# Optimization experiments

Hardware: AMD Instinct MI355X
Metric: run time of the kernel (lower is better)

The kernel has to match this reference:

```python
import jax, jax.numpy as jnp
import numpy as np

IMAGE_SIZE = 128
PATCH_SIZE = 8
BOND_DIM = 128
CP_RANK = 64
EMBED_DIM = 512
BATCH = 512
GRID = IMAGE_SIZE // PATCH_SIZE            # 16
NUM_PATCHES = GRID * GRID                  # 256
DEPTH = 4                                  # log4(256)
LEVEL_NODES = [64, 16, 4, 1]


def setup_inputs() -> dict:
    key = jax.random.key(0)
    ks = jax.random.split(key, 32)
    s = 0.02
    inp = {
        "x": jax.random.normal(ks[0], (BATCH, 1, IMAGE_SIZE, IMAGE_SIZE), jnp.float32),
        "W_patch": jax.random.normal(ks[1], (PATCH_SIZE * PATCH_SIZE, BOND_DIM), jnp.float32) * s,
        "b_patch": jnp.zeros((BOND_DIM,), jnp.float32),
        "pos": jax.random.normal(ks[2], (1, NUM_PATCHES, BOND_DIM), jnp.float32),
        "gamma": jnp.ones((BOND_DIM,), jnp.float32),
        "beta": jnp.zeros((BOND_DIM,), jnp.float32),
        "W_head": jax.random.normal(ks[3], (BOND_DIM, EMBED_DIM), jnp.float32) * s,
        "b_head": jnp.zeros((EMBED_DIM,), jnp.float32),
    }
    for lvl, n in enumerate(LEVEL_NODES):
        # per-node distinct CP factors: 4 children in_dim->rank, then rank->out_dim
        inp[f"f{lvl}"] = jax.random.normal(ks[4 + 2 * lvl], (n, 4, BOND_DIM, CP_RANK), jnp.float32) * s
        inp[f"o{lvl}"] = jax.random.normal(ks[5 + 2 * lvl], (n, CP_RANK, BOND_DIM), jnp.float32) * s
    return inp


def _patchify(x):
    # 'b c (h p1) (w p2) -> b (h w) (p1 p2 c)', c == 1
    b = x.shape[0]
    x = x.reshape(b, 1, GRID, PATCH_SIZE, GRID, PATCH_SIZE)
    x = x.transpose(0, 2, 4, 3, 5, 1)                  # b h w p1 p2 c
    return x.reshape(b, NUM_PATCHES, PATCH_SIZE * PATCH_SIZE)


def _quad_group(x, grid):
    # 'b (h w) c -> b (h/2 w/2) (h2 w2) c' with 2x2 blocks
    b, _, c = x.shape
    g2 = grid // 2
    x = x.reshape(b, g2, 2, g2, 2, c).transpose(0, 1, 3, 2, 4, 5)
    return x.reshape(b, g2 * g2, 4, c)


def _cp_level(x, f, o):
    # x: [b, n, 4, C]; f: [n, 4, C, R]; o: [n, R, C]
    u = jnp.einsum('bnqc,nqcr->bnqr', x, f)
    p = jnp.prod(u, axis=2)                            # [b, n, R]
    return jnp.einsum('bnr,nrc->bnc', p, o)


def reference(x, W_patch, b_patch, pos, f0, o0, f1, o1, f2, o2, f3, o3,
              gamma, beta, W_head, b_head):
    h = _patchify(x) @ W_patch + b_patch               # [b, 256, C]
    h = h + pos
    grid = GRID
    for f, o in ((f0, o0), (f1, o1), (f2, o2), (f3, o3)):
        h = _cp_level(_quad_group(h, grid), f, o)
        grid //= 2
    h = h[:, 0, :]                                     # squeeze node dim
    mu = jnp.mean(h, axis=-1, keepdims=True)
    var = jnp.var(h, axis=-1, keepdims=True)
    h = (h - mu) / jnp.sqrt(var + 1e-5) * gamma + beta
    out = h @ W_head + b_head
    n = jnp.maximum(jnp.linalg.norm(out, axis=-1, keepdims=True), 1e-12)
    return out / n
```

## Files before the change

kernel.cpp:

```cpp
#include <hip/hip_runtime.h>
#include <hip/hip_bf16.h>

#define BATCH     512
#define IMG       128
#define PS        8
#define GRID_P    16
#define NP        256
#define C         128
#define R         64
#define E         512

typedef float f32x4 __attribute__((ext_vector_type(4)));
typedef short s16x8 __attribute__((ext_vector_type(8)));

__device__ __forceinline__ unsigned short f2bf(float x) {
    unsigned int u = __float_as_uint(x);
    u += 0x7fffu + ((u >> 16) & 1u);
    return (unsigned short)(u >> 16);
}
__device__ __forceinline__ float bf2f(unsigned short h) {
    return __uint_as_float(((unsigned int)h) << 16);
}

__global__ __launch_bounds__(256) void prep_all_kernel(
    const float* __restrict__ f0, const float* __restrict__ f1,
    const float* __restrict__ f2, const float* __restrict__ f3,
    const float* __restrict__ o0, const float* __restrict__ o1,
    const float* __restrict__ o2, const float* __restrict__ o3,
    const float* __restrict__ Wh, const float* __restrict__ Wp,
    const float* __restrict__ pos, const float* __restrict__ bp,
    unsigned short* __restrict__ fTL, unsigned short* __restrict__ oT,
    unsigned short* __restrict__ WhT, unsigned short* __restrict__ WfT,
    float* __restrict__ pf)
{
    __shared__ float ls[128 * 68];
    __shared__ float red[64 * 4];
    const int bi = blockIdx.x, t = threadIdx.x;

    if (bi < 256) {
        const float* src = f0 + (size_t)bi * 8192;
#pragma unroll
        for (int i = 0; i < 8; ++i) {
            const int fi = (t + 256 * i) * 4;
            const int c = fi >> 6, r = fi & 63;
            *(float4*)(ls + c * 68 + r) = *(const float4*)(src + fi);
        }
        __syncthreads();

        const int w = t >> 6, lane = t & 63;
        const int m = lane & 15, g = lane >> 4;

        f32x4 acc[4];
#pragma unroll
        for (int nt = 0; nt < 4; ++nt) acc[nt] = (f32x4){0.f, 0.f, 0.f, 0.f};
#pragma unroll
        for (int kt = 0; kt < 4; ++kt) {
            s16x8 afr;
#pragma unroll
            for (int e = 0; e < 8; ++e)
                afr[e] = (short)f2bf(ls[(kt * 32 + g * 8 + e) * 68 + w * 16 + m]);
#pragma unroll
            for (int nt = 0; nt < 4; ++nt) {
                const float* wr = Wp + (size_t)(nt * 16 + m) * 128 + kt * 32 + g * 8;
                const float4 b0 = *(const float4*)wr;
                const float4 b1 = *(const float4*)(wr + 4);
                s16x8 bfr;
                bfr[0] = (short)f2bf(b0.x); bfr[1] = (short)f2bf(b0.y);
                bfr[2] = (short)f2bf(b0.z); bfr[3] = (short)f2bf(b0.w);
                bfr[4] = (short)f2bf(b1.x); bfr[5] = (short)f2bf(b1.y);
                bfr[6] = (short)f2bf(b1.z); bfr[7] = (short)f2bf(b1.w);
                acc[nt] = __builtin_amdgcn_mfma_f32_16x16x32_bf16(afr, bfr, acc[nt], 0, 0, 0);
            }
        }
        unsigned short* D = WfT + (size_t)bi * 4096;
#pragma unroll
        for (int nt = 0; nt < 4; ++nt)
#pragma unroll
            for (int j = 0; j < 4; ++j)
                D[(size_t)(w * 16 + g * 4 + j) * 64 + nt * 16 + m] = f2bf(acc[nt][j]);

        {
            const int r = t & 63, half = t >> 6;
            const int n0 = bi >> 2, q = bi & 3;
            const int pp = (2 * (n0 >> 3) + (q >> 1)) * GRID_P + 2 * (n0 & 7) + (q & 1);
            const float* posr = pos + (size_t)pp * C;
            float s = 0.f;
#pragma unroll 8
            for (int e = 0; e < 32; ++e) {
                const int c = half * 32 + e;
                s += (posr[c] + bp[c]) * ls[c * 68 + r];
            }
            red[r * 4 + half] = s;
        }
        __syncthreads();
        if (t < 64)
            pf[bi * 64 + t] = red[t * 4 + 0] + red[t * 4 + 1] + red[t * 4 + 2] + red[t * 4 + 3];
    } else if (bi < 340) {
        const int ti = bi - 256;
        const float* src;
        if      (ti < 64) src = f1 + (size_t)ti * 8192;
        else if (ti < 80) src = f2 + (size_t)(ti - 64) * 8192;
        else              src = f3 + (size_t)(ti - 80) * 8192;
        unsigned short* dst = fTL + (size_t)ti * 8192;
#pragma unroll
        for (int i = 0; i < 8; ++i) {
            const int fi = (t + 256 * i) * 4;
            const int c = fi >> 6, r = fi & 63;
            *(float4*)(ls + c * 68 + r) = *(const float4*)(src + fi);
        }
        __syncthreads();
        const int rr = t >> 2, seg = t & 3;
        unsigned int* d32 = (unsigned int*)(dst + rr * 128 + seg * 32);
#pragma unroll
        for (int ii = 0; ii < 16; ++ii) {
            const int c = seg * 32 + ii * 2;
            const unsigned int lo = f2bf(ls[c * 68 + rr]);
            const unsigned int hi = f2bf(ls[(c + 1) * 68 + rr]);
            d32[ii] = lo | (hi << 16);
        }
    } else if (bi < 425) {
        const int oi = bi - 340;
        const float* src;
        if      (oi < 64) src = o0 + (size_t)oi * 8192;
        else if (oi < 80) src = o1 + (size_t)(oi - 64) * 8192;
        else if (oi < 84) src = o2 + (size_t)(oi - 80) * 8192;
        else              src = o3 + (size_t)(oi - 84) * 8192;
        unsigned short* dst = oT + (size_t)oi * 8192;
#pragma unroll
        for (int i = 0; i < 8; ++i) {
            const int fi = (t + 256 * i) * 4;
            const int r = fi >> 7, c = fi & 127;
            *(float4*)(ls + r * 132 + c) = *(const float4*)(src + fi);
        }
        __syncthreads();
        const int cc = t >> 1, seg = t & 1;
        unsigned int* d32 = (unsigned int*)(dst + cc * 64 + seg * 32);
#pragma unroll
        for (int ii = 0; ii < 16; ++ii) {
            const int r = seg * 32 + ii * 2;
            const unsigned int lo = f2bf(ls[r * 132 + cc]);
            const unsigned int hi = f2bf(ls[(r + 1) * 132 + cc]);
            d32[ii] = lo | (hi << 16);
        }
    } else {
        const int j = bi - 425;
#pragma unroll
        for (int i = 0; i < 8; ++i) {
            const int fi = (t + 256 * i) * 4;
            const int c = fi >> 6, e = fi & 63;
            *(float4*)(ls + c * 68 + e) = *(const float4*)(Wh + (size_t)c * E + j * 64 + e);
        }
        __syncthreads();
        const int rr = t >> 2, seg = t & 3;
        unsigned int* d32 = (unsigned int*)(WhT + (size_t)(j * 64 + rr) * 128 + seg * 32);
#pragma unroll
        for (int ii = 0; ii < 16; ++ii) {
            const int c = seg * 32 + ii * 2;
            const unsigned int lo = f2bf(ls[c * 68 + rr]);
            const unsigned int hi = f2bf(ls[(c + 1) * 68 + rr]);
            d32[ii] = lo | (hi << 16);
        }
    }
}

__global__ __launch_bounds__(256, 3) void level01_fused(
    const float* __restrict__ x,
    const unsigned short* __restrict__ WfT,
    const float* __restrict__ pf,
    const unsigned short* __restrict__ oT,
    const unsigned short* __restrict__ fT1,
    unsigned short* __restrict__ h2)
{
    __shared__ __align__(16) float          us1[4 * 16 * 68];
    __shared__ __align__(16) unsigned short ps0[4 * 16 * 72];
    __shared__ __align__(16) unsigned short ps1[16 * 72];
    __shared__ __align__(16) unsigned short h1s[4 * 16 * 136];

    const int bi = blockIdx.x;
    const int n1 = bi >> 5, btile = bi & 31;
    const int t = threadIdx.x, w = t >> 6, lane = t & 63;
    const int m = lane & 15, g = lane >> 4;
    const int bt = btile * 16;

    const int y1g = n1 >> 2, x1g = n1 & 3;
    const int Ry0 = y1g * 32, Rx0 = x1g * 32;
    const int n0 = (2 * y1g + (w >> 1)) * 8 + 2 * x1g + (w & 1);

    s16x8 a[4][2];
    {
        const int rbase = 16 * (w >> 1);
        const int cbase = 16 * (w & 1);
        const float* xb = x + (size_t)(bt + m) * (IMG * IMG);
#pragma unroll
        for (int q = 0; q < 4; ++q) {
            const int rq = rbase + 8 * (q >> 1) + g;
            const int cc = cbase + 8 * (q & 1);
#pragma unroll
            for (int kt = 0; kt < 2; ++kt) {
                const float* px = xb + (size_t)(Ry0 + rq + kt * 4) * IMG + Rx0 + cc;
                const float4 p0 = *(const float4*)px;
                const float4 p1 = *(const float4*)(px + 4);
                s16x8 fr;
                fr[0] = (short)f2bf(p0.x); fr[1] = (short)f2bf(p0.y);
                fr[2] = (short)f2bf(p0.z); fr[3] = (short)f2bf(p0.w);
                fr[4] = (short)f2bf(p1.x); fr[5] = (short)f2bf(p1.y);
                fr[6] = (short)f2bf(p1.z); fr[7] = (short)f2bf(p1.w);
                a[q][kt] = fr;
            }
        }
    }

    f32x4 accu[4][4];
#pragma unroll
    for (int q = 0; q < 4; ++q) {
        const float* pfq = pf + (size_t)(n0 * 4 + q) * 64;
#pragma unroll
        for (int nt = 0; nt < 4; ++nt) {
            const float pv = pfq[nt * 16 + m];
            accu[q][nt] = (f32x4){pv, pv, pv, pv};
        }
    }
#pragma unroll
    for (int q = 0; q < 4; ++q) {
        const unsigned short* Wq = WfT + (size_t)(n0 * 4 + q) * 4096;
#pragma unroll
        for (int kt = 0; kt < 2; ++kt) {
            const int koff = kt * 32 + g * 8;
#pragma unroll
            for (int nt = 0; nt < 4; ++nt) {
                const s16x8 bfr = *(const s16x8*)(Wq + (size_t)(nt * 16 + m) * 64 + koff);
                accu[q][nt] = __builtin_amdgcn_mfma_f32_16x16x32_bf16(a[q][kt], bfr, accu[q][nt], 0, 0, 0);
            }
        }
    }

    unsigned short* myps = ps0 + w * (16 * 72);
#pragma unroll
    for (int nt = 0; nt < 4; ++nt) {
        const f32x4 pr = accu[0][nt] * accu[1][nt] * accu[2][nt] * accu[3][nt];
#pragma unroll
        for (int j = 0; j < 4; ++j)
            myps[(g * 4 + j) * 72 + nt * 16 + m] = f2bf(pr[j]);
    }

    {
        s16x8 ap[2];
#pragma unroll
        for (int kt = 0; kt < 2; ++kt)
            ap[kt] = *(const s16x8*)(myps + m * 72 + kt * 32 + g * 8);
        const unsigned short* oTn = oT + (size_t)n0 * 8192;
        unsigned short* myh = h1s + w * (16 * 136);
#pragma unroll
        for (int ct = 0; ct < 8; ++ct) {
            f32x4 aco = (f32x4){0.f, 0.f, 0.f, 0.f};
#pragma unroll
            for (int kt = 0; kt < 2; ++kt) {
                const s16x8 bfr = *(const s16x8*)(oTn + (size_t)(ct * 16 + m) * 64 + kt * 32 + g * 8);
                aco = __builtin_amdgcn_mfma_f32_16x16x32_bf16(ap[kt], bfr, aco, 0, 0, 0);
            }
#pragma unroll
            for (int j = 0; j < 4; ++j)
                myh[(g * 4 + j) * 136 + ct * 16 + m] = f2bf(aco[j]);
        }
    }

    {
        const unsigned short* myh = h1s + w * (16 * 136);
        const unsigned short* fq = fT1 + (size_t)(n1 * 4 + w) * 8192;
        f32x4 au[4];
#pragma unroll
        for (int nt = 0; nt < 4; ++nt) au[nt] = (f32x4){0.f, 0.f, 0.f, 0.f};
#pragma unroll
        for (int kt = 0; kt < 4; ++kt) {
            const int koff = kt * 32 + g * 8;
            const s16x8 afr = *(const s16x8*)(myh + m * 136 + koff);
#pragma unroll
            for (int nt = 0; nt < 4; ++nt) {
                const s16x8 bfr = *(const s16x8*)(fq + (size_t)(nt * 16 + m) * 128 + koff);
                au[nt] = __builtin_amdgcn_mfma_f32_16x16x32_bf16(afr, bfr, au[nt], 0, 0, 0);
            }
        }
#pragma unroll
        for (int nt = 0; nt < 4; ++nt)
#pragma unroll
            for (int j = 0; j < 4; ++j)
                us1[(w * 16 + g * 4 + j) * 68 + nt * 16 + m] = au[nt][j];
    }
    __syncthreads();

    {
        const int pb = t >> 4, r0 = (t & 15) * 4;
        const f32x4 u0 = *(const f32x4*)(us1 + (0 * 16 + pb) * 68 + r0);
        const f32x4 u1 = *(const f32x4*)(us1 + (1 * 16 + pb) * 68 + r0);
        const f32x4 u2 = *(const f32x4*)(us1 + (2 * 16 + pb) * 68 + r0);
        const f32x4 u3 = *(const f32x4*)(us1 + (3 * 16 + pb) * 68 + r0);
        const f32x4 p = u0 * u1 * u2 * u3;
        uint2 v;
        v.x = (unsigned int)f2bf(p[0]) | ((unsigned int)f2bf(p[1]) << 16);
        v.y = (unsigned int)f2bf(p[2]) | ((unsigned int)f2bf(p[3]) << 16);
        *(uint2*)(ps1 + pb * 72 + r0) = v;
    }
    __syncthreads();

    {
        s16x8 ap[2];
#pragma unroll
        for (int kt = 0; kt < 2; ++kt)
            ap[kt] = *(const s16x8*)(ps1 + m * 72 + kt * 32 + g * 8);
        const unsigned short* oTn = oT + (size_t)(64 + n1) * 8192;
#pragma unroll
        for (int i = 0; i < 2; ++i) {
            const int ct = w * 2 + i;
            f32x4 aco = (f32x4){0.f, 0.f, 0.f, 0.f};
#pragma unroll
            for (int kt = 0; kt < 2; ++kt) {
                const s16x8 bfr = *(const s16x8*)(oTn + (size_t)(ct * 16 + m) * 64 + kt * 32 + g * 8);
                aco = __builtin_amdgcn_mfma_f32_16x16x32_bf16(ap[kt], bfr, aco, 0, 0, 0);
            }
#pragma unroll
            for (int j = 0; j < 4; ++j)
                h2[((size_t)(bt + g * 4 + j) * 16 + n1) * C + ct * 16 + m] = f2bf(aco[j]);
        }
    }
}

__global__ __launch_bounds__(256, 1) void tail_kernel(
    const unsigned short* __restrict__ h2,
    const unsigned short* __restrict__ fT2,
    const unsigned short* __restrict__ oT2,
    const unsigned short* __restrict__ fT3,
    const unsigned short* __restrict__ oT3,
    const float* __restrict__ gamma, const float* __restrict__ beta,
    const unsigned short* __restrict__ WhT,
    const float* __restrict__ bh,
    float* __restrict__ out)
{
    __shared__ __align__(16) float          us3[4 * 16 * 68];
    __shared__ __align__(16) unsigned short ps2[4 * 16 * 72];
    __shared__ __align__(16) unsigned short ps3[16 * 72];
    __shared__ __align__(16) unsigned short h3s[16 * 4 * 136];
    __shared__ __align__(16) float          h4s[16 * 132];
    __shared__ __align__(16) unsigned short hns[16 * 136];
    __shared__ float red[16 * 4];

    const int bt = blockIdx.x * 16;
    const int t = threadIdx.x, w = t >> 6, lane = t & 63;
    const int m = lane & 15, g = lane >> 4;

    {
        const int n2 = w;
        const int y1 = n2 >> 1, x1 = n2 & 1;

        s16x8 xa[4][4];
#pragma unroll
        for (int q = 0; q < 4; ++q) {
            const int pidx = (2 * y1 + (q >> 1)) * 4 + 2 * x1 + (q & 1);
            const unsigned short* xq = h2 + ((size_t)(bt + m) * 16 + pidx) * C;
#pragma unroll
            for (int kt = 0; kt < 4; ++kt)
                xa[q][kt] = *(const s16x8*)(xq + kt * 32 + g * 8);
        }

        f32x4 acc_u[4][4];
#pragma unroll
        for (int q = 0; q < 4; ++q)
#pragma unroll
            for (int nt = 0; nt < 4; ++nt) acc_u[q][nt] = (f32x4){0.f, 0.f, 0.f, 0.f};
#pragma unroll
        for (int q = 0; q < 4; ++q) {
            const unsigned short* fq = fT2 + (size_t)(n2 * 4 + q) * R * C;
#pragma unroll
            for (int kt = 0; kt < 4; ++kt) {
                const int koff = kt * 32 + g * 8;
#pragma unroll
                for (int nt = 0; nt < 4; ++nt) {
                    const s16x8 bfr = *(const s16x8*)(fq + (size_t)(nt * 16 + m) * C + koff);
                    acc_u[q][nt] = __builtin_amdgcn_mfma_f32_16x16x32_bf16(xa[q][kt], bfr, acc_u[q][nt], 0, 0, 0);
                }
            }
        }

        s16x8 ob[8][2];
        {
            const unsigned short* oTn = oT2 + (size_t)n2 * C * R;
#pragma unroll
            for (int ct = 0; ct < 8; ++ct)
#pragma unroll
                for (int kt = 0; kt < 2; ++kt)
                    ob[ct][kt] = *(const s16x8*)(oTn + (size_t)(ct * 16 + m) * R + kt * 32 + g * 8);
        }

        unsigned short* myps2 = ps2 + w * 16 * 72;
#pragma unroll
        for (int nt = 0; nt < 4; ++nt) {
            const f32x4 p = acc_u[0][nt] * acc_u[1][nt] * acc_u[2][nt] * acc_u[3][nt];
#pragma unroll
            for (int j = 0; j < 4; ++j)
                myps2[(g * 4 + j) * 72 + nt * 16 + m] = f2bf(p[j]);
        }
        f32x4 aco[8];
#pragma unroll
        for (int ct = 0; ct < 8; ++ct) aco[ct] = (f32x4){0.f, 0.f, 0.f, 0.f};
#pragma unroll
        for (int kt = 0; kt < 2; ++kt) {
            const int koff = kt * 32 + g * 8;
            const s16x8 av = *(const s16x8*)(myps2 + m * 72 + koff);
#pragma unroll
            for (int ct = 0; ct < 8; ++ct)
                aco[ct] = __builtin_amdgcn_mfma_f32_16x16x32_bf16(av, ob[ct][kt], aco[ct], 0, 0, 0);
        }
#pragma unroll
        for (int ct = 0; ct < 8; ++ct)
#pragma unroll
            for (int j = 0; j < 4; ++j)
                h3s[((g * 4 + j) * 4 + n2) * 136 + ct * 16 + m] = f2bf(aco[ct][j]);
    }
    __syncthreads();

    {
        const int q = w;
        s16x8 fb[4][4];
        {
            const unsigned short* fq = fT3 + (size_t)q * R * C;
#pragma unroll
            for (int kt = 0; kt < 4; ++kt)
#pragma unroll
                for (int nt = 0; nt < 4; ++nt)
                    fb[kt][nt] = *(const s16x8*)(fq + (size_t)(nt * 16 + m) * C + kt * 32 + g * 8);
        }
        f32x4 acc_u[4];
#pragma unroll
        for (int nt = 0; nt < 4; ++nt) acc_u[nt] = (f32x4){0.f, 0.f, 0.f, 0.f};
#pragma unroll
        for (int kt = 0; kt < 4; ++kt) {
            const int koff = kt * 32 + g * 8;
            const s16x8 av = *(const s16x8*)(h3s + (m * 4 + q) * 136 + koff);
#pragma unroll
            for (int nt = 0; nt < 4; ++nt)
                acc_u[nt] = __builtin_amdgcn_mfma_f32_16x16x32_bf16(av, fb[kt][nt], acc_u[nt], 0, 0, 0);
        }
#pragma unroll
        for (int nt = 0; nt < 4; ++nt)
#pragma unroll
            for (int j = 0; j < 4; ++j)
                us3[(q * 16 + g * 4 + j) * 68 + nt * 16 + m] = acc_u[nt][j];
    }
    __syncthreads();
    {
        const int pb = t >> 4, r0 = (t & 15) * 4;
        const f32x4 u0 = *(const f32x4*)(us3 + (0 * 16 + pb) * 68 + r0);
        const f32x4 u1 = *(const f32x4*)(us3 + (1 * 16 + pb) * 68 + r0);
        const f32x4 u2 = *(const f32x4*)(us3 + (2 * 16 + pb) * 68 + r0);
        const f32x4 u3 = *(const f32x4*)(us3 + (3 * 16 + pb) * 68 + r0);
        const f32x4 p = u0 * u1 * u2 * u3;
        uint2 v;
        v.x = (unsigned int)f2bf(p[0]) | ((unsigned int)f2bf(p[1]) << 16);
        v.y = (unsigned int)f2bf(p[2]) | ((unsigned int)f2bf(p[3]) << 16);
        *(uint2*)(ps3 + pb * 72 + r0) = v;
    }
    __syncthreads();
    {
        s16x8 ap[2];
#pragma unroll
        for (int kt = 0; kt < 2; ++kt)
            ap[kt] = *(const s16x8*)(ps3 + m * 72 + kt * 32 + g * 8);
#pragma unroll
        for (int i = 0; i < 2; ++i) {
            f32x4 aco = (f32x4){0.f, 0.f, 0.f, 0.f};
            const int ct = w * 2 + i;
#pragma unroll
            for (int kt = 0; kt < 2; ++kt) {
                const s16x8 bfr = *(const s16x8*)(oT3 + (size_t)(ct * 16 + m) * R + kt * 32 + g * 8);
                aco = __builtin_amdgcn_mfma_f32_16x16x32_bf16(ap[kt], bfr, aco, 0, 0, 0);
            }
#pragma unroll
            for (int j = 0; j < 4; ++j)
                h4s[(g * 4 + j) * 132 + ct * 16 + m] = aco[j];
        }
    }
    __syncthreads();

    {
        const int rb = w * 4 + g;
        const int c0 = m * 8;
        const f32x4 v0 = *(const f32x4*)(h4s + rb * 132 + c0);
        const f32x4 v1 = *(const f32x4*)(h4s + rb * 132 + c0 + 4);
        float s  = v0[0] + v0[1] + v0[2] + v0[3] + v1[0] + v1[1] + v1[2] + v1[3];
        float ss = v0[0]*v0[0] + v0[1]*v0[1] + v0[2]*v0[2] + v0[3]*v0[3]
                 + v1[0]*v1[0] + v1[1]*v1[1] + v1[2]*v1[2] + v1[3]*v1[3];
#pragma unroll
        for (int off = 1; off < 16; off <<= 1) {
            s  += __shfl_xor(s, off);
            ss += __shfl_xor(ss, off);
        }
        const float mu   = s * (1.f / C);
        const float var  = ss * (1.f / C) - mu * mu;
        const float rstd = rsqrtf(var + 1e-5f);
        const f32x4 ga0 = *(const f32x4*)(gamma + c0);
        const f32x4 ga1 = *(const f32x4*)(gamma + c0 + 4);
        const f32x4 be0 = *(const f32x4*)(beta + c0);
        const f32x4 be1 = *(const f32x4*)(beta + c0 + 4);
        unsigned int o32[4];
        float hv[8];
#pragma unroll
        for (int k = 0; k < 4; ++k) hv[k]     = (v0[k] - mu) * rstd * ga0[k] + be0[k];
#pragma unroll
        for (int k = 0; k < 4; ++k) hv[4 + k] = (v1[k] - mu) * rstd * ga1[k] + be1[k];
#pragma unroll
        for (int k = 0; k < 4; ++k)
            o32[k] = (unsigned int)f2bf(hv[2*k]) | ((unsigned int)f2bf(hv[2*k+1]) << 16);
        *(uint4*)(hns + rb * 136 + c0) = *(uint4*)o32;
    }
    __syncthreads();

    {
        f32x4 acc[8];
#pragma unroll
        for (int nt = 0; nt < 8; ++nt) {
            const int e = w * 128 + nt * 16 + m;
            const float bv = bh[e];
            acc[nt] = (f32x4){bv, bv, bv, bv};
        }
#pragma unroll
        for (int kt = 0; kt < 4; ++kt) {
            const int koff = kt * 32 + g * 8;
            const s16x8 av = *(const s16x8*)(hns + m * 136 + koff);
#pragma unroll
            for (int nt = 0; nt < 8; ++nt) {
                const int e = w * 128 + nt * 16 + m;
                const s16x8 bfr = *(const s16x8*)(WhT + (size_t)e * 128 + koff);
                acc[nt] = __builtin_amdgcn_mfma_f32_16x16x32_bf16(av, bfr, acc[nt], 0, 0, 0);
            }
        }
        float sq[4];
#pragma unroll
        for (int j = 0; j < 4; ++j) {
            float s = 0.f;
#pragma unroll
            for (int nt = 0; nt < 8; ++nt) s += acc[nt][j] * acc[nt][j];
#pragma unroll
            for (int off = 1; off < 16; off <<= 1) s += __shfl_xor(s, off);
            sq[j] = s;
        }
        if (m == 0) {
#pragma unroll
            for (int j = 0; j < 4; ++j) red[(g * 4 + j) * 4 + w] = sq[j];
        }
        __syncthreads();
#pragma unroll
        for (int j = 0; j < 4; ++j) {
            const int row = g * 4 + j;
            const float tot = red[row * 4 + 0] + red[row * 4 + 1]
                            + red[row * 4 + 2] + red[row * 4 + 3];
            const float inv = 1.f / fmaxf(sqrtf(tot), 1e-12f);
#pragma unroll
            for (int nt = 0; nt < 8; ++nt) {
                const int e = w * 128 + nt * 16 + m;
                out[(size_t)(bt + row) * E + e] = acc[nt][j] * inv;
            }
        }
    }
}

extern "C" void kernel_launch(void* const* d_in, const int* in_sizes, int n_in,
                              void* d_out, int out_size, void* d_ws, size_t ws_size,
                              hipStream_t stream) {
    const float* x     = (const float*)d_in[0];
    const float* Wp    = (const float*)d_in[1];
    const float* bp    = (const float*)d_in[2];
    const float* pos   = (const float*)d_in[3];
    const float* gamma = (const float*)d_in[4];
    const float* beta  = (const float*)d_in[5];
    const float* Wh    = (const float*)d_in[6];
    const float* bh    = (const float*)d_in[7];
    const float* f0    = (const float*)d_in[8];
    const float* o0    = (const float*)d_in[9];
    const float* f1    = (const float*)d_in[10];
    const float* o1    = (const float*)d_in[11];
    const float* f2    = (const float*)d_in[12];
    const float* o2    = (const float*)d_in[13];
    const float* f3    = (const float*)d_in[14];
    const float* o3    = (const float*)d_in[15];
    float* out = (float*)d_out;

    unsigned short* h2  = (unsigned short*)d_ws;
    unsigned short* fTL = h2 + (size_t)1048576;
    unsigned short* oT  = fTL + (size_t)688128;
    unsigned short* WfT = oT + (size_t)696320;
    unsigned short* WhT = WfT + (size_t)1048576;
    float*          pff = (float*)(WhT + 65536);

    unsigned short* fT1 = fTL;
    unsigned short* fT2 = fTL + (size_t)64 * 8192;
    unsigned short* fT3 = fTL + (size_t)80 * 8192;
    unsigned short* oT2 = oT + (size_t)80 * 8192;
    unsigned short* oT3 = oT + (size_t)84 * 8192;

    prep_all_kernel<<<433, 256, 0, stream>>>(f0, f1, f2, f3, o0, o1, o2, o3,
                                             Wh, Wp, pos, bp,
                                             fTL, oT, WhT, WfT, pff);

    level01_fused<<<16 * 32, 256, 0, stream>>>(x, WfT, pff, oT, fT1, h2);

    tail_kernel<<<32, 256, 0, stream>>>(h2, fT2, oT2, fT3, oT3,
                                        gamma, beta, WhT, bh, out);
}
```

Measured before the change: 155.9 us.

## Merge prep, level01 and tail kernels into one cooperative kernel with grid syncs

Replaces the three kernel launches with a single cooperative launch of 512 blocks, using grid.sync() between the weight-prep phase, the fused level 0/1 phase and the tail phase. Input pixel loads are hoisted ahead of the prep work so they overlap it. The aim is to remove launch overhead and the gaps between kernels. In exchange, occupancy is capped at 2 blocks per CU by the shared-memory union and launch bounds, grid-wide barriers carry their own cost, and the tail phase runs on only 32 blocks while the rest exit.

```diff
diff --git a/kernel.cpp b/kernel.cpp
--- a/kernel.cpp
+++ b/kernel.cpp
@@ -1,5 +1,8 @@
 #include <hip/hip_runtime.h>
 #include <hip/hip_bf16.h>
+#include <hip/hip_cooperative_groups.h>
+
+namespace cg = cooperative_groups;
 
 #define BATCH     512
 #define IMG       128
@@ -18,24 +21,80 @@
     u += 0x7fffu + ((u >> 16) & 1u);
     return (unsigned short)(u >> 16);
 }
-__device__ __forceinline__ float bf2f(unsigned short h) {
-    return __uint_as_float(((unsigned int)h) << 16);
-}
-
-__global__ __launch_bounds__(256) void prep_all_kernel(
-    const float* __restrict__ f0, const float* __restrict__ f1,
-    const float* __restrict__ f2, const float* __restrict__ f3,
-    const float* __restrict__ o0, const float* __restrict__ o1,
-    const float* __restrict__ o2, const float* __restrict__ o3,
-    const float* __restrict__ Wh, const float* __restrict__ Wp,
-    const float* __restrict__ pos, const float* __restrict__ bp,
-    unsigned short* __restrict__ fTL, unsigned short* __restrict__ oT,
-    unsigned short* __restrict__ WhT, unsigned short* __restrict__ WfT,
-    float* __restrict__ pf)
+
+__global__ __launch_bounds__(256, 2) void mega_kernel(
+    const float* __restrict__ x,     const float* __restrict__ Wp,
+    const float* __restrict__ bp,    const float* __restrict__ pos,
+    const float* __restrict__ gamma, const float* __restrict__ beta,
+    const float* __restrict__ Wh,    const float* __restrict__ bh,
+    const float* __restrict__ f0,    const float* __restrict__ o0,
+    const float* __restrict__ f1,    const float* __restrict__ o1,
+    const float* __restrict__ f2,    const float* __restrict__ o2,
+    const float* __restrict__ f3,    const float* __restrict__ o3,
+    unsigned short* __restrict__ ws, float* __restrict__ out)
 {
-    __shared__ float ls[128 * 68];
-    __shared__ float red[64 * 4];
+    unsigned short* h2  = ws;
+    unsigned short* fTL = h2 + (size_t)1048576;
+    unsigned short* oT  = fTL + (size_t)688128;
+    unsigned short* WfT = oT + (size_t)696320;
+    unsigned short* WhT = WfT + (size_t)1048576;
+    float*          pf  = (float*)(WhT + 65536);
+    unsigned short* fT1 = fTL;
+    unsigned short* fT2 = fTL + (size_t)64 * 8192;
+    unsigned short* fT3 = fTL + (size_t)80 * 8192;
+    unsigned short* oT2 = oT + (size_t)80 * 8192;
+    unsigned short* oT3 = oT + (size_t)84 * 8192;
+
+    __shared__ __align__(16) char smem[59392];
+    float*          ls   = (float*)         (smem);
+    float*          redp = (float*)         (smem + 34816);
+    float*          us1  = (float*)         (smem);
+    unsigned short* ps0  = (unsigned short*)(smem + 17408);
+    unsigned short* ps1  = (unsigned short*)(smem + 26624);
+    unsigned short* h1s  = (unsigned short*)(smem + 28928);
+    float*          us3  = (float*)         (smem);
+    unsigned short* ps2  = (unsigned short*)(smem + 17408);
+    unsigned short* ps3  = (unsigned short*)(smem + 26624);
+    unsigned short* h3s  = (unsigned short*)(smem + 28928);
+    float*          h4s  = (float*)         (smem + 46336);
+    unsigned short* hns  = (unsigned short*)(smem + 54784);
+    float*          redt = (float*)         (smem + 59136);
+
+    cg::grid_group grid = cg::this_grid();
+
     const int bi = blockIdx.x, t = threadIdx.x;
+    const int w = t >> 6, lane = t & 63;
+    const int m = lane & 15, g = lane >> 4;
+
+    const int n1 = bi >> 5, btile = bi & 31;
+    const int btL = btile * 16;
+    const int y1g = n1 >> 2, x1g = n1 & 3;
+    const int Ry0 = y1g * 32, Rx0 = x1g * 32;
+    const int n0 = (2 * y1g + (w >> 1)) * 8 + 2 * x1g + (w & 1);
+
+    s16x8 a[4][2];
+    {
+        const int rbase = 16 * (w >> 1);
+        const int cbase = 16 * (w & 1);
+        const float* xb = x + (size_t)(btL + m) * (IMG * IMG);
+#pragma unroll
+        for (int q = 0; q < 4; ++q) {
+            const int rq = rbase + 8 * (q >> 1) + g;
+            const int cc = cbase + 8 * (q & 1);
+#pragma unroll
+            for (int kt = 0; kt < 2; ++kt) {
+                const float* px = xb + (size_t)(Ry0 + rq + kt * 4) * IMG + Rx0 + cc;
+                const float4 p0 = *(const float4*)px;
+                const float4 p1 = *(const float4*)(px + 4);
+                s16x8 fr;
+                fr[0] = (short)f2bf(p0.x); fr[1] = (short)f2bf(p0.y);
+                fr[2] = (short)f2bf(p0.z); fr[3] = (short)f2bf(p0.w);
+                fr[4] = (short)f2bf(p1.x); fr[5] = (short)f2bf(p1.y);
+                fr[6] = (short)f2bf(p1.z); fr[7] = (short)f2bf(p1.w);
+                a[q][kt] = fr;
+            }
+        }
+    }
 
     if (bi < 256) {
         const float* src = f0 + (size_t)bi * 8192;
@@ -46,9 +105,6 @@
             *(float4*)(ls + c * 68 + r) = *(const float4*)(src + fi);
         }
         __syncthreads();
-
-        const int w = t >> 6, lane = t & 63;
-        const int m = lane & 15, g = lane >> 4;
 
         f32x4 acc[4];
 #pragma unroll
@@ -81,8 +137,8 @@
 
         {
             const int r = t & 63, half = t >> 6;
-            const int n0 = bi >> 2, q = bi & 3;
-            const int pp = (2 * (n0 >> 3) + (q >> 1)) * GRID_P + 2 * (n0 & 7) + (q & 1);
+            const int nn = bi >> 2, q = bi & 3;
+            const int pp = (2 * (nn >> 3) + (q >> 1)) * GRID_P + 2 * (nn & 7) + (q & 1);
             const float* posr = pos + (size_t)pp * C;
             float s = 0.f;
 #pragma unroll 8
@@ -90,11 +146,11 @@
                 const int c = half * 32 + e;
                 s += (posr[c] + bp[c]) * ls[c * 68 + r];
             }
-            red[r * 4 + half] = s;
+            redp[r * 4 + half] = s;
         }
         __syncthreads();
         if (t < 64)
-            pf[bi * 64 + t] = red[t * 4 + 0] + red[t * 4 + 1] + red[t * 4 + 2] + red[t * 4 + 3];
+            pf[bi * 64 + t] = redp[t * 4 + 0] + redp[t * 4 + 1] + redp[t * 4 + 2] + redp[t * 4 + 3];
     } else if (bi < 340) {
         const int ti = bi - 256;
         const float* src;
@@ -142,7 +198,7 @@
             const unsigned int hi = f2bf(ls[(r + 1) * 132 + cc]);
             d32[ii] = lo | (hi << 16);
         }
-    } else {
+    } else if (bi < 433) {
         const int j = bi - 425;
 #pragma unroll
         for (int i = 0; i < 8; ++i) {
@@ -161,191 +217,128 @@
             d32[ii] = lo | (hi << 16);
         }
     }
-}
-
-__global__ __launch_bounds__(256, 3) void level01_fused(
-    const float* __restrict__ x,
-    const unsigned short* __restrict__ WfT,
-    const float* __restrict__ pf,
-    const unsigned short* __restrict__ oT,
-    const unsigned short* __restrict__ fT1,
-    unsigned short* __restrict__ h2)
-{
-    __shared__ __align__(16) float          us1[4 * 16 * 68];
-    __shared__ __align__(16) unsigned short ps0[4 * 16 * 72];
-    __shared__ __align__(16) unsigned short ps1[16 * 72];
-    __shared__ __align__(16) unsigned short h1s[4 * 16 * 136];
-
-    const int bi = blockIdx.x;
-    const int n1 = bi >> 5, btile = bi & 31;
-    const int t = threadIdx.x, w = t >> 6, lane = t & 63;
-    const int m = lane & 15, g = lane >> 4;
-    const int bt = btile * 16;
-
-    const int y1g = n1 >> 2, x1g = n1 & 3;
-    const int Ry0 = y1g * 32, Rx0 = x1g * 32;
-    const int n0 = (2 * y1g + (w >> 1)) * 8 + 2 * x1g + (w & 1);
-
-    s16x8 a[4][2];
-    {
-        const int rbase = 16 * (w >> 1);
-        const int cbase = 16 * (w & 1);
-        const float* xb = x + (size_t)(bt + m) * (IMG * IMG);
+
+    grid.sync();
+
+    {
+        f32x4 accu[4][4];
 #pragma unroll
         for (int q = 0; q < 4; ++q) {
-            const int rq = rbase + 8 * (q >> 1) + g;
-            const int cc = cbase + 8 * (q & 1);
+            const float* pfq = pf + (size_t)(n0 * 4 + q) * 64;
+#pragma unroll
+            for (int nt = 0; nt < 4; ++nt) {
+                const float pv = pfq[nt * 16 + m];
+                accu[q][nt] = (f32x4){pv, pv, pv, pv};
+            }
+        }
+#pragma unroll
+        for (int q = 0; q < 4; ++q) {
+            const unsigned short* Wq = WfT + (size_t)(n0 * 4 + q) * 4096;
 #pragma unroll
             for (int kt = 0; kt < 2; ++kt) {
-                const float* px = xb + (size_t)(Ry0 + rq + kt * 4) * IMG + Rx0 + cc;
-                const float4 p0 = *(const float4*)px;
-                const float4 p1 = *(const float4*)(px + 4);
-                s16x8 fr;
-                fr[0] = (short)f2bf(p0.x); fr[1] = (short)f2bf(p0.y);
-                fr[2] = (short)f2bf(p0.z); fr[3] = (short)f2bf(p0.w);
-                fr[4] = (short)f2bf(p1.x); fr[5] = (short)f2bf(p1.y);
-                fr[6] = (short)f2bf(p1.z); fr[7] = (short)f2bf(p1.w);
-                a[q][kt] = fr;
-            }
-        }
-    }
-
-    f32x4 accu[4][4];
-#pragma unroll
-    for (int q = 0; q < 4; ++q) {
-        const float* pfq = pf + (size_t)(n0 * 4 + q) * 64;
+                const int koff = kt * 32 + g * 8;
+#pragma unroll
+                for (int nt = 0; nt < 4; ++nt) {
+                    const s16x8 bfr = *(const s16x8*)(Wq + (size_t)(nt * 16 + m) * 64 + koff);
+                    accu[q][nt] = __builtin_amdgcn_mfma_f32_16x16x32_bf16(a[q][kt], bfr, accu[q][nt], 0, 0, 0);
+                }
+            }
+        }
+
+        unsigned short* myps = ps0 + w * (16 * 72);
 #pragma unroll
         for (int nt = 0; nt < 4; ++nt) {
-            const float pv = pfq[nt * 16 + m];
-            accu[q][nt] = (f32x4){pv, pv, pv, pv};
-        }
-    }
-#pragma unroll
-    for (int q = 0; q < 4; ++q) {
-        const unsigned short* Wq = WfT + (size_t)(n0 * 4 + q) * 4096;
-#pragma unroll
-        for (int kt = 0; kt < 2; ++kt) {
-            const int koff = kt * 32 + g * 8;
-#pragma unroll
-            for (int nt = 0; nt < 4; ++nt) {
-                const s16x8 bfr = *(const s16x8*)(Wq + (size_t)(nt * 16 + m) * 64 + koff);
-                accu[q][nt] = __builtin_amdgcn_mfma_f32_16x16x32_bf16(a[q][kt], bfr, accu[q][nt], 0, 0, 0);
-            }
-        }
-    }
-
-    unsigned short* myps = ps0 + w * (16 * 72);
-#pragma unroll
-    for (int nt = 0; nt < 4; ++nt) {
-        const f32x4 pr = accu[0][nt] * accu[1][nt] * accu[2][nt] * accu[3][nt];
-#pragma unroll
-        for (int j = 0; j < 4; ++j)
-            myps[(g * 4 + j) * 72 + nt * 16 + m] = f2bf(pr[j]);
-    }
-
-    {
-        s16x8 ap[2];
-#pragma unroll
-        for (int kt = 0; kt < 2; ++kt)
-            ap[kt] = *(const s16x8*)(myps + m * 72 + kt * 32 + g * 8);
-        const unsigned short* oTn = oT + (size_t)n0 * 8192;
-        unsigned short* myh = h1s + w * (16 * 136);
-#pragma unroll
-        for (int ct = 0; ct < 8; ++ct) {
-            f32x4 aco = (f32x4){0.f, 0.f, 0.f, 0.f};
-#pragma unroll
-            for (int kt = 0; kt < 2; ++kt) {
-                const s16x8 bfr = *(const s16x8*)(oTn + (size_t)(ct * 16 + m) * 64 + kt * 32 + g * 8);
-                aco = __builtin_amdgcn_mfma_f32_16x16x32_bf16(ap[kt], bfr, aco, 0, 0, 0);
-            }
+            const f32x4 pr = accu[0][nt] * accu[1][nt] * accu[2][nt] * accu[3][nt];
 #pragma unroll
             for (int j = 0; j < 4; ++j)
-                myh[(g * 4 + j) * 136 + ct * 16 + m] = f2bf(aco[j]);
-        }
-    }
-
-    {
-        const unsigned short* myh = h1s + w * (16 * 136);
-        const unsigned short* fq = fT1 + (size_t)(n1 * 4 + w) * 8192;
-        f32x4 au[4];
-#pragma unroll
-        for (int nt = 0; nt < 4; ++nt) au[nt] = (f32x4){0.f, 0.f, 0.f, 0.f};
-#pragma unroll
-        for (int kt = 0; kt < 4; ++kt) {
-            const int koff = kt * 32 + g * 8;
-            const s16x8 afr = *(const s16x8*)(myh + m * 136 + koff);
-#pragma unroll
-            for (int nt = 0; nt < 4; ++nt) {
-                const s16x8 bfr = *(const s16x8*)(fq + (size_t)(nt * 16 + m) * 128 + koff);
-                au[nt] = __builtin_amdgcn_mfma_f32_16x16x32_bf16(afr, bfr, au[nt], 0, 0, 0);
-            }
-        }
-#pragma unroll
-        for (int nt = 0; nt < 4; ++nt)
-#pragma unroll
-            for (int j = 0; j < 4; ++j)
-                us1[(w * 16 + g * 4 + j) * 68 + nt * 16 + m] = au[nt][j];
-    }
-    __syncthreads();
-
-    {
-        const int pb = t >> 4, r0 = (t & 15) * 4;
-        const f32x4 u0 = *(const f32x4*)(us1 + (0 * 16 + pb) * 68 + r0);
-        const f32x4 u1 = *(const f32x4*)(us1 + (1 * 16 + pb) * 68 + r0);
-        const f32x4 u2 = *(const f32x4*)(us1 + (2 * 16 + pb) * 68 + r0);
-        const f32x4 u3 = *(const f32x4*)(us1 + (3 * 16 + pb) * 68 + r0);
-        const f32x4 p = u0 * u1 * u2 * u3;
-        uint2 v;
-        v.x = (unsigned int)f2bf(p[0]) | ((unsigned int)f2bf(p[1]) << 16);
-        v.y = (unsigned int)f2bf(p[2]) | ((unsigned int)f2bf(p[3]) << 16);
-        *(uint2*)(ps1 + pb * 72 + r0) = v;
-    }
-    __syncthreads();
-
-    {
-        s16x8 ap[2];
-#pragma unroll
-        for (int kt = 0; kt < 2; ++kt)
-            ap[kt] = *(const s16x8*)(ps1 + m * 72 + kt * 32 + g * 8);
-        const unsigned short* oTn = oT + (size_t)(64 + n1) * 8192;
-#pragma unroll
-        for (int i = 0; i < 2; ++i) {
-            const int ct = w * 2 + i;
-            f32x4 aco = (f32x4){0.f, 0.f, 0.f, 0.f};
-#pragma unroll
-            for (int kt = 0; kt < 2; ++kt) {
-                const s16x8 bfr = *(const s16x8*)(oTn + (size_t)(ct * 16 + m) * 64 + kt * 32 + g * 8);
-                aco = __builtin_amdgcn_mfma_f32_16x16x32_bf16(ap[kt], bfr, aco, 0, 0, 0);
-            }
-#pragma unroll
-            for (int j = 0; j < 4; ++j)
-                h2[((size_t)(bt + g * 4 + j) * 16 + n1) * C + ct * 16 + m] = f2bf(aco[j]);
-        }
-    }
-}
-
-__global__ __launch_bounds__(256, 1) void tail_kernel(
-    const unsigned short* __restrict__ h2,
-    const unsigned short* __restrict__ fT2,
-    const unsigned short* __restrict__ oT2,
-    const unsigned short* __restrict__ fT3,
-    const unsigned short* __restrict__ oT3,
-    const float* __restrict__ gamma, const float* __restrict__ beta,
-    const unsigned short* __restrict__ WhT,
-    const float* __restrict__ bh,
-    float* __restrict__ out)
-{
-    __shared__ __align__(16) float          us3[4 * 16 * 68];
-    __shared__ __align__(16) unsigned short ps2[4 * 16 * 72];
-    __shared__ __align__(16) unsigned short ps3[16 * 72];
-    __shared__ __align__(16) unsigned short h3s[16 * 4 * 136];
-    __shared__ __align__(16) float          h4s[16 * 132];
-    __shared__ __align__(16) unsigned short hns[16 * 136];
-    __shared__ float red[16 * 4];
-
-    const int bt = blockIdx.x * 16;
-    const int t = threadIdx.x, w = t >> 6, lane = t & 63;
-    const int m = lane & 15, g = lane >> 4;
+                myps[(g * 4 + j) * 72 + nt * 16 + m] = f2bf(pr[j]);
+        }
+
+        {
+            s16x8 ap[2];
+#pragma unroll
+            for (int kt = 0; kt < 2; ++kt)
+                ap[kt] = *(const s16x8*)(myps + m * 72 + kt * 32 + g * 8);
+            const unsigned short* oTn = oT + (size_t)n0 * 8192;
+            unsigned short* myh = h1s + w * (16 * 136);
+#pragma unroll
+            for (int ct = 0; ct < 8; ++ct) {
+                f32x4 aco = (f32x4){0.f, 0.f, 0.f, 0.f};
+#pragma unroll
+                for (int kt = 0; kt < 2; ++kt) {
+                    const s16x8 bfr = *(const s16x8*)(oTn + (size_t)(ct * 16 + m) * 64 + kt * 32 + g * 8);
+                    aco = __builtin_amdgcn_mfma_f32_16x16x32_bf16(ap[kt], bfr, aco, 0, 0, 0);
+                }
+#pragma unroll
+                for (int j = 0; j < 4; ++j)
+                    myh[(g * 4 + j) * 136 + ct * 16 + m] = f2bf(aco[j]);
+            }
+        }
+
+        {
+            const unsigned short* myh = h1s + w * (16 * 136);
+            const unsigned short* fq = fT1 + (size_t)(n1 * 4 + w) * 8192;
+            f32x4 au[4];
+#pragma unroll
+            for (int nt = 0; nt < 4; ++nt) au[nt] = (f32x4){0.f, 0.f, 0.f, 0.f};
+#pragma unroll
+            for (int kt = 0; kt < 4; ++kt) {
+                const int koff = kt * 32 + g * 8;
+                const s16x8 afr = *(const s16x8*)(myh + m * 136 + koff);
+#pragma unroll
+                for (int nt = 0; nt < 4; ++nt) {
+                    const s16x8 bfr = *(const s16x8*)(fq + (size_t)(nt * 16 + m) * 128 + koff);
+                    au[nt] = __builtin_amdgcn_mfma_f32_16x16x32_bf16(afr, bfr, au[nt], 0, 0, 0);
+                }
+            }
+#pragma unroll
+            for (int nt = 0; nt < 4; ++nt)
+#pragma unroll
+                for (int j = 0; j < 4; ++j)
+                    us1[(w * 16 + g * 4 + j) * 68 + nt * 16 + m] = au[nt][j];
+        }
+        __syncthreads();
+
+        {
+            const int pb = t >> 4, r0 = (t & 15) * 4;
+            const f32x4 u0 = *(const f32x4*)(us1 + (0 * 16 + pb) * 68 + r0);
+            const f32x4 u1 = *(const f32x4*)(us1 + (1 * 16 + pb) * 68 + r0);
+            const f32x4 u2 = *(const f32x4*)(us1 + (2 * 16 + pb) * 68 + r0);
+            const f32x4 u3 = *(const f32x4*)(us1 + (3 * 16 + pb) * 68 + r0);
+            const f32x4 p = u0 * u1 * u2 * u3;
+            uint2 v;
+            v.x = (unsigned int)f2bf(p[0]) | ((unsigned int)f2bf(p[1]) << 16);
+            v.y = (unsigned int)f2bf(p[2]) | ((unsigned int)f2bf(p[3]) << 16);
+            *(uint2*)(ps1 + pb * 72 + r0) = v;
+        }
+        __syncthreads();
+
+        {
+            s16x8 ap[2];
+#pragma unroll
+            for (int kt = 0; kt < 2; ++kt)
+                ap[kt] = *(const s16x8*)(ps1 + m * 72 + kt * 32 + g * 8);
+            const unsigned short* oTn = oT + (size_t)(64 + n1) * 8192;
+#pragma unroll
+            for (int i = 0; i < 2; ++i) {
+                const int ct = w * 2 + i;
+                f32x4 aco = (f32x4){0.f, 0.f, 0.f, 0.f};
+#pragma unroll
+                for (int kt = 0; kt < 2; ++kt) {
+                    const s16x8 bfr = *(const s16x8*)(oTn + (size_t)(ct * 16 + m) * 64 + kt * 32 + g * 8);
+                    aco = __builtin_amdgcn_mfma_f32_16x16x32_bf16(ap[kt], bfr, aco, 0, 0, 0);
+                }
+#pragma unroll
+                for (int j = 0; j < 4; ++j)
+                    h2[((size_t)(btL + g * 4 + j) * 16 + n1) * C + ct * 16 + m] = f2bf(aco[j]);
+            }
+        }
+    }
+
+    grid.sync();
+
+    if (bi >= 32) return;
+    const int bt = bi * 16;
 
     {
         const int n2 = w;
@@ -544,14 +537,14 @@
         }
         if (m == 0) {
 #pragma unroll
-            for (int j = 0; j < 4; ++j) red[(g * 4 + j) * 4 + w] = sq[j];
+            for (int j = 0; j < 4; ++j) redt[(g * 4 + j) * 4 + w] = sq[j];
         }
         __syncthreads();
 #pragma unroll
         for (int j = 0; j < 4; ++j) {
             const int row = g * 4 + j;
-            const float tot = red[row * 4 + 0] + red[row * 4 + 1]
-                            + red[row * 4 + 2] + red[row * 4 + 3];
+            const float tot = redt[row * 4 + 0] + redt[row * 4 + 1]
+                            + redt[row * 4 + 2] + redt[row * 4 + 3];
             const float inv = 1.f / fmaxf(sqrtf(tot), 1e-12f);
 #pragma unroll
             for (int nt = 0; nt < 8; ++nt) {
@@ -581,27 +574,16 @@
     const float* o2    = (const float*)d_in[13];
     const float* f3    = (const float*)d_in[14];
     const float* o3    = (const float*)d_in[15];
+    unsigned short* ws = (unsigned short*)d_ws;
     float* out = (float*)d_out;
 
-    unsigned short* h2  = (unsigned short*)d_ws;
-    unsigned short* fTL = h2 + (size_t)1048576;
-    unsigned short* oT  = fTL + (size_t)688128;
-    unsigned short* WfT = oT + (size_t)696320;
-    unsigned short* WhT = WfT + (size_t)1048576;
-    float*          pff = (float*)(WhT + 65536);
-
-    unsigned short* fT1 = fTL;
-    unsigned short* fT2 = fTL + (size_t)64 * 8192;
-    unsigned short* fT3 = fTL + (size_t)80 * 8192;
-    unsigned short* oT2 = oT + (size_t)80 * 8192;
-    unsigned short* oT3 = oT + (size_t)84 * 8192;
-
-    prep_all_kernel<<<433, 256, 0, stream>>>(f0, f1, f2, f3, o0, o1, o2, o3,
-                                             Wh, Wp, pos, bp,
-                                             fTL, oT, WhT, WfT, pff);
-
-    level01_fused<<<16 * 32, 256, 0, stream>>>(x, WfT, pff, oT, fT1, h2);
-
-    tail_kernel<<<32, 256, 0, stream>>>(h2, fT2, oT2, fT3, oT3,
-                                        gamma, beta, WhT, bh, out);
+    void* kargs[] = {
+        (void*)&x, (void*)&Wp, (void*)&bp, (void*)&pos,
+        (void*)&gamma, (void*)&beta, (void*)&Wh, (void*)&bh,
+        (void*)&f0, (void*)&o0, (void*)&f1, (void*)&o1,
+        (void*)&f2, (void*)&o2, (void*)&f3, (void*)&o3,
+        (void*)&ws, (void*)&out
+    };
+    hipLaunchCooperativeKernel((const void*)mega_kernel,
+                               dim3(512), dim3(256), kargs, 0, stream);
 }
```

Result: slower. 303.5 us (+94.6%).
